# Kernel optimization log

Measured on AMD Instinct MI355X. Metric: run time of the kernel, lower is better.

## Reference

```python
import jax, jax.numpy as jnp
import numpy as np

NUM_GROUPS = 17
NUM_OCCLUDED = 10
TEMP = 0.1


def setup_inputs() -> dict:
    key = jax.random.key(0)
    k1, k2 = jax.random.split(key)
    B, N, D = 128, 577, 768
    x = jax.random.normal(k1, (B, N, D), dtype=jnp.float32)
    # xavier_uniform-like scale for (D, G) weight
    bound = float(np.sqrt(6.0 / (D + NUM_GROUPS)))
    group_weights = jax.random.uniform(k2, (D, NUM_GROUPS), dtype=jnp.float32, minval=-bound, maxval=bound)
    return {"x": x, "group_weights": group_weights}


def _l2_normalize(v):
    # matches F.normalize(dim=-1, eps=1e-12)
    return v / jnp.maximum(jnp.linalg.norm(v, axis=-1, keepdims=True), 1e-12)


def reference(x, group_weights):
    B, N, D = x.shape
    cls_token = x[:, 0, :]            # (B, D)
    patch_tokens = x[:, 1:, :]        # (B, P, D), P = N-1

    # cosine similarity of each patch with cls token
    sim = jnp.einsum('bpd,bd->bp', _l2_normalize(patch_tokens), _l2_normalize(cls_token))  # (B, P)

    # k least-similar patches are "occluded" -> zero them out
    _, occ_idx = jax.lax.top_k(-sim, NUM_OCCLUDED)  # (B, K)
    mask = jnp.ones_like(sim).at[jnp.arange(B)[:, None], occ_idx].set(0.0)  # (B, P)
    non_occ = patch_tokens * mask[..., None]  # (B, P, D)

    # attention-style group pooling; softmax over groups (dim=1)
    scores = jnp.einsum('dg,bpd->bgp', group_weights, non_occ) / TEMP  # (B, G, P)
    attn = jax.nn.softmax(scores, axis=1)
    group_features = jnp.einsum('bgp,bpd->bgd', attn, non_occ)  # (B, G, D)

    # pack [global_feat, group_feat_1..G] as (B, 1+G, D)
    feats = jnp.concatenate([cls_token[:, None, :], group_features], axis=1)
    return feats, attn
```

## Files before the change

kernel.cpp:

```cpp
#include <hip/hip_runtime.h>
#include <math.h>

#define B_ 128
#define NTOK 577
#define P_ 576
#define D_ 768
#define G_ 17
#define KOCC 10
#define INV_TEMP 10.0f
#define U17 (1.0f / 17.0f)
#define NCHUNK 9

#define OFF_WT 0
#define OFF_SIM (G_ * D_)
#define OFF_CLSINV (OFF_SIM + B_ * P_)
#define OFF_GFP (OFF_CLSINV + B_)
#define GFP_PART ((size_t)B_ * G_ * D_)

__global__ __launch_bounds__(256) void k0_cls(const float* __restrict__ x,
                                              const float* __restrict__ gw,
                                              float* __restrict__ feats,
                                              float* __restrict__ clsinv,
                                              float* __restrict__ wt,
                                              int zero_groups) {
    if (blockIdx.x >= B_) {
        int g = blockIdx.x - B_;
        for (int d = threadIdx.x; d < D_; d += 256)
            wt[g * D_ + d] = gw[d * G_ + g];
        return;
    }
    int b = blockIdx.x;
    const float* cls = x + (size_t)b * NTOK * D_;
    float* fb = feats + (size_t)b * 18 * D_;
    float ss = 0.f;
    for (int i = threadIdx.x; i < D_ / 4; i += 256) {
        float4 v = ((const float4*)cls)[i];
        ((float4*)fb)[i] = v;
        ss = fmaf(v.x, v.x, fmaf(v.y, v.y, fmaf(v.z, v.z, fmaf(v.w, v.w, ss))));
    }
    if (zero_groups) {
        float4 z = {0.f, 0.f, 0.f, 0.f};
        for (int i = threadIdx.x; i < G_ * D_ / 4; i += 256)
            ((float4*)(fb + D_))[i] = z;
    }
    #pragma unroll
    for (int off = 32; off; off >>= 1) ss += __shfl_xor(ss, off, 64);
    __shared__ float red[4];
    int wave = threadIdx.x >> 6, lane = threadIdx.x & 63;
    if (lane == 0) red[wave] = ss;
    __syncthreads();
    if (threadIdx.x == 0) {
        float t = red[0] + red[1] + red[2] + red[3];
        clsinv[b] = 1.0f / fmaxf(sqrtf(t), 1e-12f);
    }
}

__global__ __launch_bounds__(512) void k13_score_pv(const float* __restrict__ x,
                                                    const float* __restrict__ wt,
                                                    const float* __restrict__ clsinv,
                                                    float* __restrict__ sim,
                                                    float* __restrict__ attn,
                                                    float* __restrict__ gfp,
                                                    float* __restrict__ feats,
                                                    int use_part) {
    __shared__ __align__(16) float wlds[G_ * D_];
    __shared__ __align__(16) float clds[D_];
    __shared__ __align__(16) float atile[19 * 68];

    int tid = threadIdx.x;
    int b = blockIdx.y, chunk = blockIdx.x;
    const float* clsrow = x + (size_t)b * NTOK * D_;

    int lane = tid & 63, wave = tid >> 6;
    int lr = lane & 15, rh = lane >> 4;
    int lr4 = lr * 4;
    int pbase = wave * 8 + rh * 2;
    const float* xp0 = x + ((size_t)(b * NTOK + 1 + chunk * 64 + pbase)) * D_ + lr4;

    float4 xv[2], xn[2];
    xv[0] = *(const float4*)(xp0);
    xv[1] = *(const float4*)(xp0 + D_);

    for (int i = tid; i < G_ * D_ / 4; i += 512)
        ((float4*)wlds)[i] = ((const float4*)wt)[i];
    for (int i = tid; i < D_ / 4; i += 512)
        ((float4*)clds)[i] = ((const float4*)clsrow)[i];

    float s[19][2];
    #pragma unroll
    for (int i = 0; i < 19; ++i) { s[i][0] = 0.f; s[i][1] = 0.f; }

    xn[0] = xv[0]; xn[1] = xv[1];
    __syncthreads();

    for (int kc = 0; kc < 12; ++kc) {
        if (kc < 11) {
            xn[0] = *(const float4*)(xp0 + (kc + 1) * 64);
            xn[1] = *(const float4*)(xp0 + (kc + 1) * 64 + D_);
        }
        float4 cls4 = *(const float4*)&clds[kc * 64 + lr4];
        const float* wk = wlds + kc * 64 + lr4;
        #pragma unroll
        for (int g = 0; g < 17; ++g) {
            float4 w4 = *(const float4*)(wk + (size_t)g * D_);
            #pragma unroll
            for (int m = 0; m < 2; ++m)
                s[g][m] = fmaf(xv[m].x, w4.x, fmaf(xv[m].y, w4.y,
                          fmaf(xv[m].z, w4.z, fmaf(xv[m].w, w4.w, s[g][m]))));
        }
        #pragma unroll
        for (int m = 0; m < 2; ++m)
            s[17][m] = fmaf(xv[m].x, cls4.x, fmaf(xv[m].y, cls4.y,
                       fmaf(xv[m].z, cls4.z, fmaf(xv[m].w, cls4.w, s[17][m]))));
        #pragma unroll
        for (int m = 0; m < 2; ++m)
            s[18][m] = fmaf(xv[m].x, xv[m].x, fmaf(xv[m].y, xv[m].y,
                       fmaf(xv[m].z, xv[m].z, fmaf(xv[m].w, xv[m].w, s[18][m]))));
        xv[0] = xn[0]; xv[1] = xn[1];
    }

    #pragma unroll
    for (int off = 8; off >= 1; off >>= 1)
        #pragma unroll
        for (int i = 0; i < 19; ++i)
            #pragma unroll
            for (int m = 0; m < 2; ++m)
                s[i][m] += __shfl_xor(s[i][m], off, 16);

    #pragma unroll
    for (int g = 0; g < 19; ++g) {
        if (lr == ((g < 16) ? g : 15)) {
            float2 v = {s[g][0], s[g][1]};
            *(float2*)&atile[g * 68 + pbase] = v;
        }
    }
    __syncthreads();

    if (tid < 64) {
        int p = chunk * 64 + tid;
        float v[17];
        float mx = -3.0e38f;
        #pragma unroll
        for (int g = 0; g < 17; ++g) {
            v[g] = atile[g * 68 + tid];
            mx = fmaxf(mx, v[g]);
        }
        float tot = 0.f;
        #pragma unroll
        for (int g = 0; g < 17; ++g) {
            v[g] = __expf((v[g] - mx) * INV_TEMP);
            tot += v[g];
        }
        float inv = 1.0f / tot;
        float* ap = attn + ((size_t)b * G_) * P_ + p;
        #pragma unroll
        for (int g = 0; g < 17; ++g) {
            float av = v[g] * inv;
            ap[(size_t)g * P_] = av;
            atile[g * 68 + tid] = av;
        }
        float cd = atile[17 * 68 + tid];
        float sq = atile[18 * 68 + tid];
        sim[(size_t)b * P_ + p] = cd * clsinv[b] / fmaxf(sqrtf(sq), 1e-12f);
    }
    __syncthreads();

    if (tid >= 192) return;
    const float* xb = x + ((size_t)(b * NTOK) + 1 + chunk * 64) * D_ + tid * 4;
    float4 acc[G_];
    #pragma unroll
    for (int g = 0; g < G_; ++g) acc[g] = make_float4(0.f, 0.f, 0.f, 0.f);

    float4 c0 = *(const float4*)(xb + (size_t)0 * D_);
    float4 c1 = *(const float4*)(xb + (size_t)1 * D_);
    float4 c2 = *(const float4*)(xb + (size_t)2 * D_);
    float4 c3 = *(const float4*)(xb + (size_t)3 * D_);

    for (int pp = 0; pp < 64; pp += 4) {
        float4 n0 = c0, n1 = c1, n2 = c2, n3 = c3;
        if (pp + 4 < 64) {
            n0 = *(const float4*)(xb + (size_t)(pp + 4) * D_);
            n1 = *(const float4*)(xb + (size_t)(pp + 5) * D_);
            n2 = *(const float4*)(xb + (size_t)(pp + 6) * D_);
            n3 = *(const float4*)(xb + (size_t)(pp + 7) * D_);
        }
        #pragma unroll
        for (int g = 0; g < G_; ++g) {
            float4 a = *(const float4*)&atile[g * 68 + pp];
            acc[g].x = fmaf(a.x, c0.x, fmaf(a.y, c1.x, fmaf(a.z, c2.x, fmaf(a.w, c3.x, acc[g].x))));
            acc[g].y = fmaf(a.x, c0.y, fmaf(a.y, c1.y, fmaf(a.z, c2.y, fmaf(a.w, c3.y, acc[g].y))));
            acc[g].z = fmaf(a.x, c0.z, fmaf(a.y, c1.z, fmaf(a.z, c2.z, fmaf(a.w, c3.z, acc[g].z))));
            acc[g].w = fmaf(a.x, c0.w, fmaf(a.y, c1.w, fmaf(a.z, c2.w, fmaf(a.w, c3.w, acc[g].w))));
        }
        c0 = n0; c1 = n1; c2 = n2; c3 = n3;
    }

    if (use_part) {
        float* gb = gfp + ((size_t)(chunk * B_ + b) * G_) * D_ + tid * 4;
        #pragma unroll
        for (int g = 0; g < G_; ++g) *(float4*)(gb + (size_t)g * D_) = acc[g];
    } else {
        float* fb = feats + ((size_t)(b * 18) + 1) * D_ + tid * 4;
        #pragma unroll
        for (int g = 0; g < G_; ++g) {
            atomicAdd(fb + (size_t)g * D_ + 0, acc[g].x);
            atomicAdd(fb + (size_t)g * D_ + 1, acc[g].y);
            atomicAdd(fb + (size_t)g * D_ + 2, acc[g].z);
            atomicAdd(fb + (size_t)g * D_ + 3, acc[g].w);
        }
    }
}

__global__ __launch_bounds__(192) void k24_fin(const float* __restrict__ x,
                                               const float* __restrict__ sim,
                                               const float* __restrict__ gfp,
                                               float* __restrict__ attn,
                                               float* __restrict__ feats,
                                               int use_part) {
    __shared__ int s_occ[KOCC];
    __shared__ float s_a0[KOCC][G_];
    int b = blockIdx.x, tid = threadIdx.x;

    if (tid < 64) {
        int lane = tid;
        int base = lane * 9;
        float v[9];
        #pragma unroll
        for (int j = 0; j < 9; ++j) v[j] = sim[(size_t)b * P_ + base + j];
        for (int t = 0; t < KOCC; ++t) {
            float mv = 3.0e38f;
            int mi = 1 << 30;
            #pragma unroll
            for (int j = 0; j < 9; ++j) {
                if (v[j] < mv) { mv = v[j]; mi = base + j; }
            }
            #pragma unroll
            for (int off = 1; off < 64; off <<= 1) {
                float ov = __shfl_xor(mv, off, 64);
                int oi = __shfl_xor(mi, off, 64);
                if (ov < mv || (ov == mv && oi < mi)) { mv = ov; mi = oi; }
            }
            if (lane == 0) s_occ[t] = mi;
            int loc = mi - base;
            if (loc >= 0 && loc < 9) v[loc] = 3.0e38f;
        }
    }

    float4 acc[G_];
    float* fb = feats + ((size_t)(b * 18) + 1) * D_ + tid * 4;
    if (use_part) {
        #pragma unroll
        for (int g = 0; g < G_; ++g) acc[g] = make_float4(0.f, 0.f, 0.f, 0.f);
        for (int pc = 0; pc < NCHUNK; ++pc) {
            const float* gb = gfp + ((size_t)(pc * B_ + b) * G_) * D_ + tid * 4;
            #pragma unroll
            for (int g = 0; g < G_; ++g) {
                float4 v = *(const float4*)(gb + (size_t)g * D_);
                acc[g].x += v.x; acc[g].y += v.y; acc[g].z += v.z; acc[g].w += v.w;
            }
        }
    } else {
        #pragma unroll
        for (int g = 0; g < G_; ++g) acc[g] = *(const float4*)(fb + (size_t)g * D_);
    }
    __syncthreads();

    for (int i = tid; i < KOCC * G_; i += 192) {
        int t = i / G_, g = i - t * G_;
        size_t idx = ((size_t)b * G_ + g) * P_ + s_occ[t];
        s_a0[t][g] = attn[idx];
        attn[idx] = U17;
    }
    __syncthreads();

    #pragma unroll
    for (int t = 0; t < KOCC; ++t) {
        float4 xo = *(const float4*)(x + ((size_t)(b * NTOK) + 1 + s_occ[t]) * D_ + tid * 4);
        #pragma unroll
        for (int g = 0; g < G_; ++g) {
            float a0 = s_a0[t][g];
            acc[g].x = fmaf(-a0, xo.x, acc[g].x);
            acc[g].y = fmaf(-a0, xo.y, acc[g].y);
            acc[g].z = fmaf(-a0, xo.z, acc[g].z);
            acc[g].w = fmaf(-a0, xo.w, acc[g].w);
        }
    }
    #pragma unroll
    for (int g = 0; g < G_; ++g) *(float4*)(fb + (size_t)g * D_) = acc[g];
}

extern "C" void kernel_launch(void* const* d_in, const int* in_sizes, int n_in,
                              void* d_out, int out_size, void* d_ws, size_t ws_size,
                              hipStream_t stream) {
    const float* x  = (const float*)d_in[0];
    const float* gw = (const float*)d_in[1];
    float* feats = (float*)d_out;
    float* attn  = (float*)d_out + (size_t)B_ * 18 * D_;
    float* wt      = (float*)d_ws + OFF_WT;
    float* sim     = (float*)d_ws + OFF_SIM;
    float* clsinv  = (float*)d_ws + OFF_CLSINV;
    float* gfp     = (float*)d_ws + OFF_GFP;

    int use_part = (((size_t)OFF_GFP + (size_t)NCHUNK * GFP_PART) * sizeof(float) <= ws_size);

    k0_cls<<<B_ + G_, 256, 0, stream>>>(x, gw, feats, clsinv, wt, !use_part);
    k13_score_pv<<<dim3(NCHUNK, B_), 512, 0, stream>>>(x, wt, clsinv, sim, attn, gfp, feats, use_part);
    k24_fin<<<B_, 192, 0, stream>>>(x, sim, gfp, attn, feats, use_part);
}
```

Before: 381.4 us.

## Drop prologue kernel, stage weights in two halves to shrink LDS

After: 762.6 us. 2x slower.

```diff
diff --git a/kernel.cpp b/kernel.cpp
--- a/kernel.cpp
+++ b/kernel.cpp
@@ -11,61 +11,26 @@
 #define U17 (1.0f / 17.0f)
 #define NCHUNK 9
 
-#define OFF_WT 0
-#define OFF_SIM (G_ * D_)
-#define OFF_CLSINV (OFF_SIM + B_ * P_)
-#define OFF_GFP (OFF_CLSINV + B_)
+#define OFF_SIM 0
+#define OFF_GFP (OFF_SIM + B_ * P_)
 #define GFP_PART ((size_t)B_ * G_ * D_)
 
-__global__ __launch_bounds__(256) void k0_cls(const float* __restrict__ x,
-                                              const float* __restrict__ gw,
-                                              float* __restrict__ feats,
-                                              float* __restrict__ clsinv,
-                                              float* __restrict__ wt,
-                                              int zero_groups) {
-    if (blockIdx.x >= B_) {
-        int g = blockIdx.x - B_;
-        for (int d = threadIdx.x; d < D_; d += 256)
-            wt[g * D_ + d] = gw[d * G_ + g];
-        return;
-    }
+__global__ __launch_bounds__(256) void kz_zero(float* __restrict__ feats) {
     int b = blockIdx.x;
-    const float* cls = x + (size_t)b * NTOK * D_;
-    float* fb = feats + (size_t)b * 18 * D_;
-    float ss = 0.f;
-    for (int i = threadIdx.x; i < D_ / 4; i += 256) {
-        float4 v = ((const float4*)cls)[i];
-        ((float4*)fb)[i] = v;
-        ss = fmaf(v.x, v.x, fmaf(v.y, v.y, fmaf(v.z, v.z, fmaf(v.w, v.w, ss))));
-    }
-    if (zero_groups) {
-        float4 z = {0.f, 0.f, 0.f, 0.f};
-        for (int i = threadIdx.x; i < G_ * D_ / 4; i += 256)
-            ((float4*)(fb + D_))[i] = z;
-    }
-    #pragma unroll
-    for (int off = 32; off; off >>= 1) ss += __shfl_xor(ss, off, 64);
-    __shared__ float red[4];
-    int wave = threadIdx.x >> 6, lane = threadIdx.x & 63;
-    if (lane == 0) red[wave] = ss;
-    __syncthreads();
-    if (threadIdx.x == 0) {
-        float t = red[0] + red[1] + red[2] + red[3];
-        clsinv[b] = 1.0f / fmaxf(sqrtf(t), 1e-12f);
-    }
+    float4 z = {0.f, 0.f, 0.f, 0.f};
+    float4* fb = (float4*)(feats + ((size_t)b * 18 + 1) * D_);
+    for (int i = threadIdx.x; i < G_ * D_ / 4; i += 256) fb[i] = z;
 }
 
 __global__ __launch_bounds__(512) void k13_score_pv(const float* __restrict__ x,
-                                                    const float* __restrict__ wt,
-                                                    const float* __restrict__ clsinv,
+                                                    const float* __restrict__ gw,
                                                     float* __restrict__ sim,
                                                     float* __restrict__ attn,
                                                     float* __restrict__ gfp,
                                                     float* __restrict__ feats,
                                                     int use_part) {
-    __shared__ __align__(16) float wlds[G_ * D_];
-    __shared__ __align__(16) float clds[D_];
-    __shared__ __align__(16) float atile[19 * 68];
+    __shared__ __align__(16) float wbuf[G_ * 384];
+    float* atile = wbuf;
 
     int tid = threadIdx.x;
     int b = blockIdx.y, chunk = blockIdx.x;
@@ -80,52 +45,77 @@
     float4 xv[2], xn[2];
     xv[0] = *(const float4*)(xp0);
     xv[1] = *(const float4*)(xp0 + D_);
-
-    for (int i = tid; i < G_ * D_ / 4; i += 512)
-        ((float4*)wlds)[i] = ((const float4*)wt)[i];
-    for (int i = tid; i < D_ / 4; i += 512)
-        ((float4*)clds)[i] = ((const float4*)clsrow)[i];
+    xn[0] = xv[0]; xn[1] = xv[1];
+
+    for (int i = tid; i < G_ * 96; i += 512) {
+        int g = i / 96, dq = i - g * 96;
+        const float* gp = gw + (size_t)(dq * 4) * G_ + g;
+        float4 w;
+        w.x = gp[0]; w.y = gp[G_]; w.z = gp[2 * G_]; w.w = gp[3 * G_];
+        *(float4*)&wbuf[g * 384 + dq * 4] = w;
+    }
 
     float s[19][2];
     #pragma unroll
     for (int i = 0; i < 19; ++i) { s[i][0] = 0.f; s[i][1] = 0.f; }
-
-    xn[0] = xv[0]; xn[1] = xv[1];
-    __syncthreads();
-
-    for (int kc = 0; kc < 12; ++kc) {
-        if (kc < 11) {
-            xn[0] = *(const float4*)(xp0 + (kc + 1) * 64);
-            xn[1] = *(const float4*)(xp0 + (kc + 1) * 64 + D_);
-        }
-        float4 cls4 = *(const float4*)&clds[kc * 64 + lr4];
-        const float* wk = wlds + kc * 64 + lr4;
-        #pragma unroll
-        for (int g = 0; g < 17; ++g) {
-            float4 w4 = *(const float4*)(wk + (size_t)g * D_);
+    float s19 = 0.f;
+
+    __syncthreads();
+
+    for (int half = 0; half < 2; ++half) {
+        if (half) {
+            __syncthreads();
+            for (int i = tid; i < G_ * 96; i += 512) {
+                int g = i / 96, dq = i - g * 96;
+                const float* gp = gw + (size_t)(384 + dq * 4) * G_ + g;
+                float4 w;
+                w.x = gp[0]; w.y = gp[G_]; w.z = gp[2 * G_]; w.w = gp[3 * G_];
+                *(float4*)&wbuf[g * 384 + dq * 4] = w;
+            }
+            __syncthreads();
+        }
+        #pragma unroll
+        for (int kc2 = 0; kc2 < 6; ++kc2) {
+            int kc = half * 6 + kc2;
+            if (kc < 11) {
+                xn[0] = *(const float4*)(xp0 + (kc + 1) * 64);
+                xn[1] = *(const float4*)(xp0 + (kc + 1) * 64 + D_);
+            }
+            float4 cls4 = *(const float4*)(clsrow + kc * 64 + lr4);
+            const float* wk = wbuf + kc2 * 64 + lr4;
+            #pragma unroll
+            for (int g = 0; g < 17; ++g) {
+                float4 w4 = *(const float4*)(wk + g * 384);
+                #pragma unroll
+                for (int m = 0; m < 2; ++m)
+                    s[g][m] = fmaf(xv[m].x, w4.x, fmaf(xv[m].y, w4.y,
+                              fmaf(xv[m].z, w4.z, fmaf(xv[m].w, w4.w, s[g][m]))));
+            }
             #pragma unroll
             for (int m = 0; m < 2; ++m)
-                s[g][m] = fmaf(xv[m].x, w4.x, fmaf(xv[m].y, w4.y,
-                          fmaf(xv[m].z, w4.z, fmaf(xv[m].w, w4.w, s[g][m]))));
-        }
-        #pragma unroll
-        for (int m = 0; m < 2; ++m)
-            s[17][m] = fmaf(xv[m].x, cls4.x, fmaf(xv[m].y, cls4.y,
-                       fmaf(xv[m].z, cls4.z, fmaf(xv[m].w, cls4.w, s[17][m]))));
-        #pragma unroll
-        for (int m = 0; m < 2; ++m)
-            s[18][m] = fmaf(xv[m].x, xv[m].x, fmaf(xv[m].y, xv[m].y,
-                       fmaf(xv[m].z, xv[m].z, fmaf(xv[m].w, xv[m].w, s[18][m]))));
-        xv[0] = xn[0]; xv[1] = xn[1];
-    }
-
-    #pragma unroll
-    for (int off = 8; off >= 1; off >>= 1)
+                s[17][m] = fmaf(xv[m].x, cls4.x, fmaf(xv[m].y, cls4.y,
+                           fmaf(xv[m].z, cls4.z, fmaf(xv[m].w, cls4.w, s[17][m]))));
+            #pragma unroll
+            for (int m = 0; m < 2; ++m)
+                s[18][m] = fmaf(xv[m].x, xv[m].x, fmaf(xv[m].y, xv[m].y,
+                           fmaf(xv[m].z, xv[m].z, fmaf(xv[m].w, xv[m].w, s[18][m]))));
+            s19 = fmaf(cls4.x, cls4.x, fmaf(cls4.y, cls4.y,
+                  fmaf(cls4.z, cls4.z, fmaf(cls4.w, cls4.w, s19))));
+            xv[0] = xn[0]; xv[1] = xn[1];
+        }
+    }
+
+    #pragma unroll
+    for (int off = 8; off >= 1; off >>= 1) {
         #pragma unroll
         for (int i = 0; i < 19; ++i)
             #pragma unroll
             for (int m = 0; m < 2; ++m)
                 s[i][m] += __shfl_xor(s[i][m], off, 16);
+        s19 += __shfl_xor(s19, off, 16);
+    }
+
+    __syncthreads();
 
     #pragma unroll
     for (int g = 0; g < 19; ++g) {
@@ -134,6 +124,10 @@
             *(float2*)&atile[g * 68 + pbase] = v;
         }
     }
+    if (lr == 15) {
+        float2 v = {s19, s19};
+        *(float2*)&atile[19 * 68 + pbase] = v;
+    }
     __syncthreads();
 
     if (tid < 64) {
@@ -161,7 +155,9 @@
         }
         float cd = atile[17 * 68 + tid];
         float sq = atile[18 * 68 + tid];
-        sim[(size_t)b * P_ + p] = cd * clsinv[b] / fmaxf(sqrtf(sq), 1e-12f);
+        float cls2 = atile[19 * 68 + tid];
+        float ci = 1.0f / fmaxf(sqrtf(cls2), 1e-12f);
+        sim[(size_t)b * P_ + p] = cd * ci / fmaxf(sqrtf(sq), 1e-12f);
     }
     __syncthreads();
 
@@ -221,6 +217,10 @@
     __shared__ float s_a0[KOCC][G_];
     int b = blockIdx.x, tid = threadIdx.x;
 
+    const float* clsrow = x + (size_t)b * NTOK * D_;
+    float* fb0 = feats + (size_t)b * 18 * D_;
+    *(float4*)(fb0 + tid * 4) = *(const float4*)(clsrow + tid * 4);
+
     if (tid < 64) {
         int lane = tid;
         int base = lane * 9;
@@ -296,14 +296,12 @@
     const float* gw = (const float*)d_in[1];
     float* feats = (float*)d_out;
     float* attn  = (float*)d_out + (size_t)B_ * 18 * D_;
-    float* wt      = (float*)d_ws + OFF_WT;
-    float* sim     = (float*)d_ws + OFF_SIM;
-    float* clsinv  = (float*)d_ws + OFF_CLSINV;
-    float* gfp     = (float*)d_ws + OFF_GFP;
+    float* sim   = (float*)d_ws + OFF_SIM;
+    float* gfp   = (float*)d_ws + OFF_GFP;
 
     int use_part = (((size_t)OFF_GFP + (size_t)NCHUNK * GFP_PART) * sizeof(float) <= ws_size);
 
-    k0_cls<<<B_ + G_, 256, 0, stream>>>(x, gw, feats, clsinv, wt, !use_part);
-    k13_score_pv<<<dim3(NCHUNK, B_), 512, 0, stream>>>(x, wt, clsinv, sim, attn, gfp, feats, use_part);
+    if (!use_part) kz_zero<<<B_, 256, 0, stream>>>(feats);
+    k13_score_pv<<<dim3(NCHUNK, B_), 512, 0, stream>>>(x, gw, sim, attn, gfp, feats, use_part);
     k24_fin<<<B_, 192, 0, stream>>>(x, sim, gfp, attn, feats, use_part);
 }
```
